# Kernel optimization log

Hardware: AMD Instinct MI355X
Metric: run time of the kernel (lower is better)

Reference implementation:

```python
import jax, jax.numpy as jnp
import numpy as np

B, S, D = 2, 2048, 4096
H, KV, HD = 32, 8, 128          # n_heads, n_kv_heads, head_dim
N_REP = H // KV                  # GQA repeat factor
THETA = 500000.0


def setup_inputs() -> dict:
    key = jax.random.key(0)
    ks = jax.random.split(key, 5)
    x = jax.random.normal(ks[0], (B, S, D), jnp.float32)
    wq = jax.random.normal(ks[1], (D, H * HD), jnp.float32) * (D ** -0.5)
    wk = jax.random.normal(ks[2], (D, KV * HD), jnp.float32) * (D ** -0.5)
    wv = jax.random.normal(ks[3], (D, KV * HD), jnp.float32) * (D ** -0.5)
    wo = jax.random.normal(ks[4], (H * HD, D), jnp.float32) * ((H * HD) ** -0.5)
    # precomputed rotary frequencies (cos/sin of freqs_cis = exp(i * pos * inv_freq))
    inv_freq = 1.0 / (THETA ** (jnp.arange(0, HD, 2, dtype=jnp.float32) / HD))
    ang = jnp.arange(S, dtype=jnp.float32)[:, None] * inv_freq[None, :]  # [S, HD/2]
    freqs_cos = jnp.cos(ang)
    freqs_sin = jnp.sin(ang)
    # causal additive mask (prefill, start_pos=0)
    mask = jnp.triu(jnp.full((S, S), -1e9, jnp.float32), k=1)
    return dict(x=x, freqs_cos=freqs_cos, freqs_sin=freqs_sin, mask=mask,
                wq=wq, wk=wk, wv=wv, wo=wo, start_pos=0)


def _rope(t, cos, sin):
    # t: [B, S, nh, HD]; complex-pair rotation on interleaved (even, odd) channels
    tr = t.reshape(*t.shape[:-1], HD // 2, 2)
    te, to = tr[..., 0], tr[..., 1]
    c = cos[None, :, None, :]
    s = sin[None, :, None, :]
    out = jnp.stack([te * c - to * s, te * s + to * c], axis=-1)
    return out.reshape(t.shape)


def reference(x, freqs_cos, freqs_sin, mask, wq, wk, wv, wo, start_pos):
    q = (x @ wq).reshape(B, S, H, HD)
    k = (x @ wk).reshape(B, S, KV, HD)
    v = (x @ wv).reshape(B, S, KV, HD)
    q = _rope(q, freqs_cos, freqs_sin)
    k = _rope(k, freqs_cos, freqs_sin)
    # prefill: cache[:, :start_pos+S] == (k, v) since start_pos == 0
    # GQA: group query heads over KV heads instead of materializing repeat_kv
    qg = q.reshape(B, S, KV, N_REP, HD)
    scores = jnp.einsum('bqgrd,bkgd->bgrqk', qg, k) / jnp.sqrt(jnp.float32(HD))
    scores = scores + mask  # broadcast [S,S] additive causal mask
    probs = jax.nn.softmax(scores.astype(jnp.float32), axis=-1).astype(q.dtype)
    out = jnp.einsum('bgrqk,bkgd->bqgrd', probs, v).reshape(B, S, H * HD)
    return out @ wo
```

## Files before the change

### kernel.cpp

```cpp
#include <hip/hip_runtime.h>

typedef unsigned short u16;
typedef unsigned int u32;

typedef __bf16 bf16x8 __attribute__((ext_vector_type(8)));
typedef float f32x4 __attribute__((ext_vector_type(4)));

#define SEQ 2048
#define NH 32
#define NKV 8
#define HDIM 128
#define QKVW 6144
#define KCOL 4096
#define VCOL 5120

__device__ __forceinline__ float b2f(u16 u) {
    return __uint_as_float(((u32)u) << 16);
}
__device__ __forceinline__ u16 f2bf(float f) {
    u32 u = __float_as_uint(f);
    u += 0x7fff + ((u >> 16) & 1);
    return (u16)(u >> 16);
}

#define GLDS16(g, l)                                                            \
    __builtin_amdgcn_global_load_lds(                                           \
        (const __attribute__((address_space(1))) void*)(g),                     \
        (__attribute__((address_space(3))) void*)(l), 16, 0, 0)

__global__ __launch_bounds__(1024) void transcvt_k(const float* __restrict__ in,
                                                   u16* __restrict__ out,
                                                   int K, int N) {
    __shared__ float tile[32][33];
    int n0 = blockIdx.x * 32, k0 = blockIdx.y * 32;
    tile[threadIdx.y][threadIdx.x] = in[(size_t)(k0 + threadIdx.y) * N + n0 + threadIdx.x];
    __syncthreads();
    out[(size_t)(n0 + threadIdx.y) * K + k0 + threadIdx.x] = f2bf(tile[threadIdx.x][threadIdx.y]);
}

__global__ __launch_bounds__(256) void cvt_k(const float* __restrict__ in,
                                             u16* __restrict__ out) {
    size_t i = ((size_t)blockIdx.x * 256 + threadIdx.x) * 8;
    float4 f0 = *(const float4*)(in + i);
    float4 f1 = *(const float4*)(in + i + 4);
    union { uint4 u4; u16 h[8]; } pk;
    pk.h[0] = f2bf(f0.x); pk.h[1] = f2bf(f0.y);
    pk.h[2] = f2bf(f0.z); pk.h[3] = f2bf(f0.w);
    pk.h[4] = f2bf(f1.x); pk.h[5] = f2bf(f1.y);
    pk.h[6] = f2bf(f1.z); pk.h[7] = f2bf(f1.w);
    *(uint4*)(out + i) = pk.u4;
}

template <bool OUT_F32>
__global__ __launch_bounds__(512, 2) void gemm256(const u16* __restrict__ A,
                                                  const u16* __restrict__ BT,
                                                  void* __restrict__ Cv,
                                                  int M, int N, int K) {
    __shared__ __align__(16) char L[131072];
    const int t = threadIdx.x, lane = t & 63, w = t >> 6;
    const int wr = w >> 2, wc = w & 3;
    const int m0 = blockIdx.y * 256, n0 = blockIdx.x * 256;
    const int r16 = lane & 15;
    const int woff = w * 1024;
    const int w8l = w * 8 + (lane >> 3);
    const int cswz = ((lane & 7) ^ (lane >> 3)) * 8;
    const u16* sA = A + (size_t)(m0 + w8l) * K + cswz;
    const u16* sB = BT + (size_t)(n0 + w8l) * K + cswz;

    const int acol0 = ((lane >> 4) * 16) ^ ((lane & 7) << 4);
    const int acol1 = (((lane >> 4) * 16) + 64) ^ ((lane & 7) << 4);
    const char* arowp = L + (wr * 128 + r16) * 128;
    const char* browp = L + 32768 + (wc * 64 + r16) * 128;

    f32x4 acc[8][4] = {};
    bf16x8 a[4][2], b0[2][2], b1[2][2];

    auto stage = [&](int bufi, int isB, int h, int kt) {
        const u16* s = isB ? sB : sA;
        char* d = (char*)L + bufi * 65536 + isB * 32768 + h * 16384 + woff;
        GLDS16(s + (size_t)(h * 128) * K + kt, d);
        GLDS16(s + (size_t)(h * 128 + 64) * K + kt, d + 8192);
    };

    const int NT = K >> 6;
    stage(0, 0, 0, 0); stage(0, 0, 1, 0); stage(0, 1, 0, 0); stage(0, 1, 1, 0);
    if (NT > 1) {
        stage(1, 0, 0, 64);
        asm volatile("s_waitcnt vmcnt(2)" ::: "memory");
    } else {
        asm volatile("s_waitcnt vmcnt(0)" ::: "memory");
    }
    __builtin_amdgcn_s_barrier();
    __builtin_amdgcn_sched_barrier(0);

    for (int T = 0; T < NT; ++T) {
        const int buf = T & 1;
        const char* Ab = arowp + buf * 65536;
        const char* Bb = browp + buf * 65536;
        const int ktn = (T + 1) << 6, ktn2 = (T + 2) << 6;

#pragma unroll
        for (int mi = 0; mi < 4; ++mi) {
            a[mi][0] = *(const bf16x8*)(Ab + mi * 2048 + acol0);
            a[mi][1] = *(const bf16x8*)(Ab + mi * 2048 + acol1);
        }
#pragma unroll
        for (int ni = 0; ni < 2; ++ni) {
            b0[ni][0] = *(const bf16x8*)(Bb + ni * 2048 + acol0);
            b0[ni][1] = *(const bf16x8*)(Bb + ni * 2048 + acol1);
        }
        if (T + 1 < NT) stage(buf ^ 1, 0, 1, ktn);
        __builtin_amdgcn_s_barrier();
        __builtin_amdgcn_sched_barrier(0);
        asm volatile("s_waitcnt lgkmcnt(0)" ::: "memory");
        __builtin_amdgcn_s_setprio(1);
#pragma unroll
        for (int mi = 0; mi < 4; ++mi)
#pragma unroll
            for (int ni = 0; ni < 2; ++ni) {
                acc[mi][ni] = __builtin_amdgcn_mfma_f32_16x16x32_bf16(a[mi][0], b0[ni][0], acc[mi][ni], 0, 0, 0);
                acc[mi][ni] = __builtin_amdgcn_mfma_f32_16x16x32_bf16(a[mi][1], b0[ni][1], acc[mi][ni], 0, 0, 0);
            }
        __builtin_amdgcn_s_setprio(0);
        __builtin_amdgcn_s_barrier();
        __builtin_amdgcn_sched_barrier(0);

#pragma unroll
        for (int ni = 0; ni < 2; ++ni) {
            b1[ni][0] = *(const bf16x8*)(Bb + (ni + 2) * 2048 + acol0);
            b1[ni][1] = *(const bf16x8*)(Bb + (ni + 2) * 2048 + acol1);
        }
        if (T + 1 < NT) stage(buf ^ 1, 1, 0, ktn);
        __builtin_amdgcn_s_barrier();
        __builtin_amdgcn_sched_barrier(0);
        asm volatile("s_waitcnt lgkmcnt(0)" ::: "memory");
        __builtin_amdgcn_s_setprio(1);
#pragma unroll
        for (int mi = 0; mi < 4; ++mi)
#pragma unroll
            for (int ni = 0; ni < 2; ++ni) {
                acc[mi][ni + 2] = __builtin_amdgcn_mfma_f32_16x16x32_bf16(a[mi][0], b1[ni][0], acc[mi][ni + 2], 0, 0, 0);
                acc[mi][ni + 2] = __builtin_amdgcn_mfma_f32_16x16x32_bf16(a[mi][1], b1[ni][1], acc[mi][ni + 2], 0, 0, 0);
            }
        __builtin_amdgcn_s_setprio(0);
        __builtin_amdgcn_s_barrier();
        __builtin_amdgcn_sched_barrier(0);

#pragma unroll
        for (int mi = 0; mi < 4; ++mi) {
            a[mi][0] = *(const bf16x8*)(Ab + (mi + 4) * 2048 + acol0);
            a[mi][1] = *(const bf16x8*)(Ab + (mi + 4) * 2048 + acol1);
        }
        if (T + 1 < NT) stage(buf ^ 1, 1, 1, ktn);
        __builtin_amdgcn_s_barrier();
        __builtin_amdgcn_sched_barrier(0);
        asm volatile("s_waitcnt lgkmcnt(0)" ::: "memory");
        __builtin_amdgcn_s_setprio(1);
#pragma unroll
        for (int mi = 0; mi < 4; ++mi)
#pragma unroll
            for (int ni = 0; ni < 2; ++ni) {
                acc[mi + 4][ni] = __builtin_amdgcn_mfma_f32_16x16x32_bf16(a[mi][0], b0[ni][0], acc[mi + 4][ni], 0, 0, 0);
                acc[mi + 4][ni] = __builtin_amdgcn_mfma_f32_16x16x32_bf16(a[mi][1], b0[ni][1], acc[mi + 4][ni], 0, 0, 0);
            }
        __builtin_amdgcn_s_setprio(0);
        __builtin_amdgcn_s_barrier();
        __builtin_amdgcn_sched_barrier(0);

        if (T + 2 < NT) stage(buf, 0, 0, ktn2);
        __builtin_amdgcn_s_setprio(1);
#pragma unroll
        for (int mi = 0; mi < 4; ++mi)
#pragma unroll
            for (int ni = 0; ni < 2; ++ni) {
                acc[mi + 4][ni + 2] = __builtin_amdgcn_mfma_f32_16x16x32_bf16(a[mi][0], b1[ni][0], acc[mi + 4][ni + 2], 0, 0, 0);
                acc[mi + 4][ni + 2] = __builtin_amdgcn_mfma_f32_16x16x32_bf16(a[mi][1], b1[ni][1], acc[mi + 4][ni + 2], 0, 0, 0);
            }
        __builtin_amdgcn_s_setprio(0);
        if (T + 2 < NT) asm volatile("s_waitcnt vmcnt(2)" ::: "memory");
        else            asm volatile("s_waitcnt vmcnt(0)" ::: "memory");
        __builtin_amdgcn_s_barrier();
        __builtin_amdgcn_sched_barrier(0);
    }

    const int r0 = (lane >> 4) * 4;
#pragma unroll
    for (int mi = 0; mi < 8; ++mi) {
#pragma unroll
        for (int r = 0; r < 4; ++r) {
            size_t row = (size_t)(m0 + wr * 128 + mi * 16 + r0 + r) * N + n0 + wc * 64;
#pragma unroll
            for (int ni = 0; ni < 4; ++ni) {
                if constexpr (OUT_F32)
                    ((float*)Cv)[row + ni * 16 + r16] = acc[mi][ni][r];
                else
                    ((u16*)Cv)[row + ni * 16 + r16] = f2bf(acc[mi][ni][r]);
            }
        }
    }
}

__global__ __launch_bounds__(256) void rope_k(u16* __restrict__ T, int col0,
                                              const float* __restrict__ cosb,
                                              const float* __restrict__ sinb,
                                              int nh) {
    int i = blockIdx.x * 256 + threadIdx.x;
    int p = i & 63;
    int h = (i >> 6) % nh;
    int bs = i / (64 * nh);
    int s = bs & (SEQ - 1);
    size_t base = (size_t)bs * QKVW + col0 + h * HDIM + 2 * p;
    ushort2 v = *(ushort2*)(T + base);
    float te = b2f(v.x), to = b2f(v.y);
    float c = cosb[s * 64 + p], sn = sinb[s * 64 + p];
    ushort2 o;
    o.x = f2bf(te * c - to * sn);
    o.y = f2bf(te * sn + to * c);
    *(ushort2*)(T + base) = o;
}

__global__ __launch_bounds__(1024) void vtrans_k(const u16* __restrict__ QKV,
                                                 u16* __restrict__ VtG) {
    __shared__ u16 tile[32][33];
    int s0 = blockIdx.x * 32, d0 = blockIdx.y * 32, plane = blockIdx.z;
    int b = plane >> 3, g = plane & 7;
    tile[threadIdx.y][threadIdx.x] =
        QKV[(size_t)(b * SEQ + s0 + threadIdx.y) * QKVW + VCOL + g * HDIM + d0 + threadIdx.x];
    __syncthreads();
    VtG[((size_t)plane * HDIM + d0 + threadIdx.y) * SEQ + s0 + threadIdx.x] =
        tile[threadIdx.x][threadIdx.y];
}

__global__ __launch_bounds__(256) void fattn_k(const u16* __restrict__ QKV,
                                               const u16* __restrict__ VtG,
                                               u16* __restrict__ O) {
    __shared__ __align__(16) char L[74752];

    const int q0 = (gridDim.x - 1 - blockIdx.x) * 64;
    const int h = blockIdx.y, b = blockIdx.z;
    const int g = h >> 2;
    const int t = threadIdx.x, lane = t & 63, w = t >> 6;
    const int row16 = lane & 15, g16 = lane >> 4;
    const int q8 = g16 * 8, q84 = g16 * 4;
    const int swz = (row16 & 7) << 4;
    const float scale = 0.08838834764831845f;

    u16* Ps = (u16*)(L + 65536) + w * (16 * 72);

    const u16* kbase = QKV + (size_t)b * SEQ * QKVW + KCOL + g * HDIM;
    const u16* vtp = VtG + (size_t)(b * NKV + g) * HDIM * SEQ;

    bf16x8 qf[4];
    {
        const u16* qptr = QKV + (size_t)(b * SEQ + q0 + w * 16 + row16) * QKVW + h * HDIM;
#pragma unroll
        for (int c = 0; c < 4; ++c) qf[c] = *(const bf16x8*)(qptr + c * 32 + q8);
    }

    const int krl = lane >> 4, kch = lane & 15;
    const int vrl = lane >> 3, vch = lane & 7;
    auto stage = [&](int bufi, int jb) {
#pragma unroll
        for (int jj = 0; jj < 4; ++jj) {
            int j = w * 4 + jj;
            int r = j * 4 + krl;
            int sc = kch ^ (r & 7);
            GLDS16(kbase + (size_t)(jb + r) * QKVW + sc * 8,
                   (char*)L + bufi * 16384 + j * 1024);
        }
#pragma unroll
        for (int jj = 0; jj < 4; ++jj) {
            int j = w * 4 + jj;
            int r = j * 8 + vrl;
            int sc = vch ^ (vrl & 7);
            GLDS16(vtp + (size_t)r * SEQ + jb + sc * 8,
                   (char*)L + 32768 + bufi * 16384 + j * 1024);
        }
    };

    f32x4 o[8];
#pragma unroll
    for (int c = 0; c < 8; ++c) o[c] = (f32x4){0.f, 0.f, 0.f, 0.f};
    float lsum[4] = {0.f, 0.f, 0.f, 0.f};

    const int NT = q0 / 64 + 1;
    stage(0, 0);
    if (NT > 1) {
        stage(1, 64);
        asm volatile("s_waitcnt vmcnt(8)" ::: "memory");
    } else {
        asm volatile("s_waitcnt vmcnt(0)" ::: "memory");
    }
    __builtin_amdgcn_s_barrier();
    __builtin_amdgcn_sched_barrier(0);

    for (int T = 0; T < NT; ++T) {
        const int jb = T * 64;
        const char* Kb = (const char*)L + (T & 1) * 16384;
        const char* Vb = (const char*)L + 32768 + (T & 1) * 16384;

#pragma unroll
        for (int sub = 0; sub < 4; ++sub) {
            f32x4 sa = {0.f, 0.f, 0.f, 0.f};
            const int srow = sub * 16 + row16;
            __builtin_amdgcn_s_setprio(1);
#pragma unroll
            for (int c = 0; c < 4; ++c) {
                bf16x8 kf = *(const bf16x8*)(Kb + srow * 256 + (((c * 4 + g16) << 4) ^ swz));
                sa = __builtin_amdgcn_mfma_f32_16x16x32_bf16(qf[c], kf, sa, 0, 0, 0);
            }
            __builtin_amdgcn_s_setprio(0);
            const int kcol = jb + sub * 16 + row16;
            const int qrow = q0 + w * 16 + q84;
#pragma unroll
            for (int r = 0; r < 4; ++r) {
                float p = (kcol <= qrow + r) ? __expf(fminf(sa[r] * scale, 80.f)) : 0.f;
                lsum[r] += p;
                Ps[(q84 + r) * 72 + sub * 16 + row16] = f2bf(p);
            }
        }
#pragma unroll
        for (int kk = 0; kk < 2; ++kk) {
            bf16x8 pf = *(const bf16x8*)(Ps + row16 * 72 + kk * 32 + q8);
            __builtin_amdgcn_s_setprio(1);
#pragma unroll
            for (int c = 0; c < 8; ++c) {
                bf16x8 vf = *(const bf16x8*)(Vb + (c * 16 + row16) * 128 + (((kk * 4 + g16) << 4) ^ swz));
                o[c] = __builtin_amdgcn_mfma_f32_16x16x32_bf16(pf, vf, o[c], 0, 0, 0);
            }
            __builtin_amdgcn_s_setprio(0);
        }

        if (T + 1 < NT) {
            __builtin_amdgcn_s_barrier();
            __builtin_amdgcn_sched_barrier(0);
            if (T + 2 < NT) {
                stage(T & 1, (T + 2) * 64);
                asm volatile("s_waitcnt vmcnt(8)" ::: "memory");
            } else {
                asm volatile("s_waitcnt vmcnt(0)" ::: "memory");
            }
            __builtin_amdgcn_s_barrier();
            __builtin_amdgcn_sched_barrier(0);
        }
    }

#pragma unroll
    for (int r = 0; r < 4; ++r)
        for (int off = 1; off < 16; off <<= 1) lsum[r] += __shfl_xor(lsum[r], off);

    float inv[4];
#pragma unroll
    for (int r = 0; r < 4; ++r) inv[r] = 1.f / lsum[r];

    u16* optr = O + (size_t)(b * SEQ + q0 + w * 16) * (NH * HDIM) + h * HDIM;
#pragma unroll
    for (int c = 0; c < 8; ++c)
#pragma unroll
        for (int r = 0; r < 4; ++r)
            optr[(size_t)(q84 + r) * (NH * HDIM) + c * 16 + row16] = f2bf(o[c][r] * inv[r]);
}

extern "C" void kernel_launch(void* const* d_in, const int* in_sizes, int n_in,
                              void* d_out, int out_size, void* d_ws, size_t ws_size,
                              hipStream_t stream) {
    const float* x    = (const float*)d_in[0];
    const float* fcos = (const float*)d_in[1];
    const float* fsin = (const float*)d_in[2];
    const float* wq = (const float*)d_in[4];
    const float* wk = (const float*)d_in[5];
    const float* wv = (const float*)d_in[6];
    const float* wo = (const float*)d_in[7];
    float* out = (float*)d_out;

    char* wsp = (char*)d_ws;
    u16* BTall = (u16*)(wsp);
    u16* VtG   = (u16*)(wsp);
    u16* woT   = (u16*)(wsp + 50331648);
    u16* xb    = (u16*)(wsp + 83886080);
    u16* ATb   = (u16*)(wsp + 83886080);
    u16* QKVb  = (u16*)(wsp + 117440512);

    const int M = 2 * SEQ;
    const int D = 4096;
    const int NQ = NH * HDIM;

    dim3 tb(32, 32);
    transcvt_k<<<dim3(4096 / 32, D / 32), tb, 0, stream>>>(wq, BTall, D, 4096);
    transcvt_k<<<dim3(1024 / 32, D / 32), tb, 0, stream>>>(wk, BTall + (size_t)4096 * 4096, D, 1024);
    transcvt_k<<<dim3(1024 / 32, D / 32), tb, 0, stream>>>(wv, BTall + (size_t)5120 * 4096, D, 1024);
    transcvt_k<<<dim3(D / 32, NQ / 32), tb, 0, stream>>>(wo, woT, NQ, D);
    cvt_k<<<(M * D) / (256 * 8), 256, 0, stream>>>(x, xb);

    gemm256<false><<<dim3(QKVW / 256, M / 256), 512, 0, stream>>>(xb, BTall, QKVb, M, QKVW, D);

    rope_k<<<(M * NH * 64) / 256, 256, 0, stream>>>(QKVb, 0, fcos, fsin, NH);
    rope_k<<<(M * NKV * 64) / 256, 256, 0, stream>>>(QKVb, KCOL, fcos, fsin, NKV);

    vtrans_k<<<dim3(SEQ / 32, HDIM / 32, 2 * NKV), tb, 0, stream>>>(QKVb, VtG);

    fattn_k<<<dim3(SEQ / 64, NH, 2), 256, 0, stream>>>(QKVb, VtG, ATb);

    gemm256<true><<<dim3(D / 256, M / 256), 512, 0, stream>>>(ATb, woT, out, M, D, NQ);

    (void)in_sizes; (void)n_in; (void)out_size; (void)ws_size;
}
```

Measured before the change: 892.7 us.

## Software-pipeline QK^T of next tile with softmax of current tile

Splits K and V staging into separate calls and computes the QK^T scores for tile T+1 before running the exp/mask softmax and PV work for tile T. The K load for tile T+2 is issued at the start of the iteration, while the V load stays after the barrier, and the wait counts are adjusted to match. The aim is to overlap matrix-core work with the VALU-bound exponent stage and to hide load latency. In exchange it holds an extra set of score registers and adds a barrier in the prologue, which may lower occupancy.

```diff
diff --git a/kernel.cpp b/kernel.cpp
--- a/kernel.cpp
+++ b/kernel.cpp
@@ -259,7 +259,7 @@
 
     const int krl = lane >> 4, kch = lane & 15;
     const int vrl = lane >> 3, vch = lane & 7;
-    auto stage = [&](int bufi, int jb) {
+    auto stageK = [&](int bufi, int jb) {
 #pragma unroll
         for (int jj = 0; jj < 4; ++jj) {
             int j = w * 4 + jj;
@@ -268,6 +268,8 @@
             GLDS16(kbase + (size_t)(jb + r) * QKVW + sc * 8,
                    (char*)L + bufi * 16384 + j * 1024);
         }
+    };
+    auto stageV = [&](int bufi, int jb) {
 #pragma unroll
         for (int jj = 0; jj < 4; ++jj) {
             int j = w * 4 + jj;
@@ -277,48 +279,58 @@
                    (char*)L + 32768 + bufi * 16384 + j * 1024);
         }
     };
+    auto qkt = [&](const char* Kb, f32x4* sa) {
+#pragma unroll
+        for (int sub = 0; sub < 4; ++sub) {
+            sa[sub] = (f32x4){0.f, 0.f, 0.f, 0.f};
+            const int srow = sub * 16 + row16;
+#pragma unroll
+            for (int c = 0; c < 4; ++c) {
+                bf16x8 kf = *(const bf16x8*)(Kb + srow * 256 + (((c * 4 + g16) << 4) ^ swz));
+                sa[sub] = __builtin_amdgcn_mfma_f32_16x16x32_bf16(qf[c], kf, sa[sub], 0, 0, 0);
+            }
+        }
+    };
 
     f32x4 o[8];
 #pragma unroll
     for (int c = 0; c < 8; ++c) o[c] = (f32x4){0.f, 0.f, 0.f, 0.f};
     float lsum[4] = {0.f, 0.f, 0.f, 0.f};
+    f32x4 scur[4], snext[4];
 
     const int NT = q0 / 64 + 1;
-    stage(0, 0);
+    stageK(0, 0); stageV(0, 0);
     if (NT > 1) {
-        stage(1, 64);
-        asm volatile("s_waitcnt vmcnt(8)" ::: "memory");
+        stageK(1, 64); stageV(1, 64);
+        asm volatile("s_waitcnt vmcnt(4)" ::: "memory");
     } else {
         asm volatile("s_waitcnt vmcnt(0)" ::: "memory");
     }
     __builtin_amdgcn_s_barrier();
     __builtin_amdgcn_sched_barrier(0);
+    qkt((const char*)L, scur);
+    __builtin_amdgcn_s_barrier();
+    __builtin_amdgcn_sched_barrier(0);
 
     for (int T = 0; T < NT; ++T) {
         const int jb = T * 64;
-        const char* Kb = (const char*)L + (T & 1) * 16384;
-        const char* Vb = (const char*)L + 32768 + (T & 1) * 16384;
+        if (T + 2 < NT) stageK(T & 1, jb + 128);
+        __builtin_amdgcn_s_setprio(1);
+        if (T + 1 < NT) qkt((const char*)L + ((T + 1) & 1) * 16384, snext);
+        __builtin_amdgcn_s_setprio(0);
 
 #pragma unroll
         for (int sub = 0; sub < 4; ++sub) {
-            f32x4 sa = {0.f, 0.f, 0.f, 0.f};
-            const int srow = sub * 16 + row16;
-            __builtin_amdgcn_s_setprio(1);
-#pragma unroll
-            for (int c = 0; c < 4; ++c) {
-                bf16x8 kf = *(const bf16x8*)(Kb + srow * 256 + (((c * 4 + g16) << 4) ^ swz));
-                sa = __builtin_amdgcn_mfma_f32_16x16x32_bf16(qf[c], kf, sa, 0, 0, 0);
-            }
-            __builtin_amdgcn_s_setprio(0);
             const int kcol = jb + sub * 16 + row16;
             const int qrow = q0 + w * 16 + q84;
 #pragma unroll
             for (int r = 0; r < 4; ++r) {
-                float p = (kcol <= qrow + r) ? __expf(fminf(sa[r] * scale, 80.f)) : 0.f;
+                float p = (kcol <= qrow + r) ? __expf(fminf(scur[sub][r] * scale, 80.f)) : 0.f;
                 lsum[r] += p;
                 Ps[(q84 + r) * 72 + sub * 16 + row16] = f2bf(p);
             }
         }
+        const char* Vb = (const char*)L + 32768 + (T & 1) * 16384;
 #pragma unroll
         for (int kk = 0; kk < 2; ++kk) {
             bf16x8 pf = *(const bf16x8*)(Ps + row16 * 72 + kk * 32 + q8);
@@ -335,14 +347,16 @@
             __builtin_amdgcn_s_barrier();
             __builtin_amdgcn_sched_barrier(0);
             if (T + 2 < NT) {
-                stage(T & 1, (T + 2) * 64);
-                asm volatile("s_waitcnt vmcnt(8)" ::: "memory");
+                stageV(T & 1, jb + 128);
+                asm volatile("s_waitcnt vmcnt(4)" ::: "memory");
             } else {
                 asm volatile("s_waitcnt vmcnt(0)" ::: "memory");
             }
             __builtin_amdgcn_s_barrier();
             __builtin_amdgcn_sched_barrier(0);
         }
+#pragma unroll
+        for (int s = 0; s < 4; ++s) scur[s] = snext[s];
     }
 
 #pragma unroll
```

Measured after the change: 879.1 us. About the same (-1.5%).
